# Kernel optimization log

Measured on AMD Instinct MI355X. Metric: run time of the kernel, lower is better.

The kernel has to match this reference:

```python
import jax, jax.numpy as jnp
import numpy as np

EPS = 1e-5
NUM_MP = 3

def _bn(x, gamma, beta):
    # eval-mode batch norm with running_mean=0, running_var=1
    return x * (gamma / jnp.sqrt(1.0 + EPS)) + beta

def _mlp(h, W1, b1, W2, b2):
    return jnp.maximum(h @ W1 + b1, 0.0) @ W2 + b2

def setup_inputs() -> dict:
    key = jax.random.key(0)
    ks = jax.random.split(key, 24)
    N, E, B, D = 50000, 800000, 16, 32
    inp = {
        'node_feats': jax.random.normal(ks[0], (N, D), jnp.float32),
        'edge_index': jax.random.randint(ks[1], (2, E), 0, N),
        'edge_feats': jax.random.normal(ks[2], (E, D), jnp.float32),
        'glob_feats': jax.random.normal(ks[3], (B, D), jnp.float32),
        'batch': jnp.sort(jax.random.randint(ks[4], (N,), 0, B)),
        'node_gamma': jax.random.uniform(ks[5], (D,), jnp.float32),
        'node_beta': jax.random.normal(ks[6], (D,), jnp.float32) * 0.1,
        'edge_gamma': jax.random.uniform(ks[7], (D,), jnp.float32),
        'edge_beta': jax.random.normal(ks[8], (D,), jnp.float32) * 0.1,
        'glob_gamma': jax.random.uniform(ks[9], (D,), jnp.float32),
        'glob_beta': jax.random.normal(ks[10], (D,), jnp.float32) * 0.1,
    }
    def w(k, shape):
        fan_in = shape[-2]
        return jax.random.normal(k, shape, jnp.float32) / np.sqrt(fan_in)
    inp['edge_W1'] = w(ks[11], (NUM_MP, 4 * D, 64)); inp['edge_b1'] = jnp.zeros((NUM_MP, 64))
    inp['edge_W2'] = w(ks[12], (NUM_MP, 64, D));     inp['edge_b2'] = jnp.zeros((NUM_MP, D))
    inp['node_W1'] = w(ks[13], (NUM_MP, 3 * D, 64)); inp['node_b1'] = jnp.zeros((NUM_MP, 64))
    inp['node_W2'] = w(ks[14], (NUM_MP, 64, D));     inp['node_b2'] = jnp.zeros((NUM_MP, D))
    inp['glob_W1'] = w(ks[15], (NUM_MP, 2 * D, 64)); inp['glob_b1'] = jnp.zeros((NUM_MP, 64))
    inp['glob_W2'] = w(ks[16], (NUM_MP, 64, D));     inp['glob_b2'] = jnp.zeros((NUM_MP, D))
    return inp

def reference(node_feats, edge_index, edge_feats, glob_feats, batch,
              node_gamma, node_beta, edge_gamma, edge_beta, glob_gamma, glob_beta,
              edge_W1, edge_b1, edge_W2, edge_b2,
              node_W1, node_b1, node_W2, node_b2,
              glob_W1, glob_b1, glob_W2, glob_b2):
    N = node_feats.shape[0]
    B = glob_feats.shape[0]
    src, dst = edge_index[0], edge_index[1]
    batch_src = batch[src]

    # input normalization
    x = _bn(node_feats, node_gamma, node_beta)
    e = _bn(edge_feats, edge_gamma, edge_beta)
    u = _bn(glob_feats, glob_gamma, glob_beta)

    # precompute mean-denominators (index structure is fixed)
    deg = jnp.maximum(jax.ops.segment_sum(jnp.ones_like(dst, jnp.float32), dst, num_segments=N), 1.0)[:, None]
    gcnt = jnp.maximum(jax.ops.segment_sum(jnp.ones_like(batch, jnp.float32), batch, num_segments=B), 1.0)[:, None]

    for l in range(NUM_MP):
        # edge model: MLP([x_src, x_dst, e, u[batch_src]])
        e_in = jnp.concatenate([x[src], x[dst], e, u[batch_src]], axis=-1)  # [E, 4D]
        e = _mlp(e_in, edge_W1[l], edge_b1[l], edge_W2[l], edge_b2[l])
        # node model: MLP([x, scatter_mean(e -> dst), u[batch]])
        agg = jax.ops.segment_sum(e, dst, num_segments=N) / deg  # [N, D]
        n_in = jnp.concatenate([x, agg, u[batch]], axis=-1)  # [N, 3D]
        x = _mlp(n_in, node_W1[l], node_b1[l], node_W2[l], node_b2[l])
        # global model: MLP([u, scatter_mean(x -> batch)])
        xg = jax.ops.segment_sum(x, batch, num_segments=B) / gcnt  # [B, D]
        g_in = jnp.concatenate([u, xg], axis=-1)  # [B, 2D]
        u = _mlp(g_in, glob_W1[l], glob_b1[l], glob_W2[l], glob_b2[l])
    return x, e, u
```

## Files before the change

kernel.cpp:

```cpp
#include <hip/hip_runtime.h>
#include <cstddef>

#define BN_RS 0.99999500003749971f

typedef __attribute__((ext_vector_type(8))) short bf16x8;
typedef __attribute__((ext_vector_type(4))) short bf16x4;
typedef __attribute__((ext_vector_type(4))) float f32x4;

#define LGKM0() asm volatile("s_waitcnt lgkmcnt(0)" ::: "memory")

__device__ __forceinline__ short f2bf(float f) {
    union { float f; unsigned u; } c; c.f = f;
    unsigned r = (c.u + 0x7fffu + ((c.u >> 16) & 1u)) >> 16;
    return (short)r;
}
__device__ __forceinline__ float bf2f(unsigned short h) {
    union { unsigned u; float f; } c; c.u = ((unsigned)h) << 16;
    return c.f;
}
__device__ __forceinline__ bf16x8 load8_bf(const float* __restrict__ p) {
    float4 a = *(const float4*)p;
    float4 b = *(const float4*)(p + 4);
    bf16x8 r;
    r[0] = f2bf(a.x); r[1] = f2bf(a.y); r[2] = f2bf(a.z); r[3] = f2bf(a.w);
    r[4] = f2bf(b.x); r[5] = f2bf(b.y); r[6] = f2bf(b.z); r[7] = f2bf(b.w);
    return r;
}

__global__ void bn_x_kernel(const float* __restrict__ in, const float* __restrict__ gamma,
                            const float* __restrict__ beta, unsigned short* __restrict__ xbf, int n4) {
    int i = blockIdx.x * blockDim.x + threadIdx.x;
    if (i >= n4) return;
    float4 v = ((const float4*)in)[i];
    float4 g = ((const float4*)gamma)[i & 7];
    float4 b = ((const float4*)beta)[i & 7];
    bf16x4 o;
    o[0] = f2bf(fmaf(v.x, g.x * BN_RS, b.x));
    o[1] = f2bf(fmaf(v.y, g.y * BN_RS, b.y));
    o[2] = f2bf(fmaf(v.z, g.z * BN_RS, b.z));
    o[3] = f2bf(fmaf(v.w, g.w * BN_RS, b.w));
    *(bf16x4*)(xbf + (size_t)i * 4) = o;
}

__global__ void bn_u_kernel(const float* __restrict__ in, const float* __restrict__ gamma,
                            const float* __restrict__ beta, float* __restrict__ ubuf,
                            unsigned short* __restrict__ ubf, int n4) {
    int i = blockIdx.x * blockDim.x + threadIdx.x;
    if (i >= n4) return;
    float4 v = ((const float4*)in)[i];
    float4 g = ((const float4*)gamma)[i & 7];
    float4 b = ((const float4*)beta)[i & 7];
    v.x = fmaf(v.x, g.x * BN_RS, b.x);
    v.y = fmaf(v.y, g.y * BN_RS, b.y);
    v.z = fmaf(v.z, g.z * BN_RS, b.z);
    v.w = fmaf(v.w, g.w * BN_RS, b.w);
    ((float4*)ubuf)[i] = v;
    bf16x4 o;
    o[0] = f2bf(v.x); o[1] = f2bf(v.y); o[2] = f2bf(v.z); o[3] = f2bf(v.w);
    *(bf16x4*)(ubf + (size_t)i * 4) = o;
}

__global__ void hist_kernel(const int* __restrict__ idx, int* __restrict__ cnt, int n) {
    int i = blockIdx.x * blockDim.x + threadIdx.x;
    if (i < n) atomicAdd(&cnt[idx[i]], 1);
}

__global__ void scan_kernel(const int* __restrict__ cnt, int* __restrict__ row, int N) {
    __shared__ int sd[1024];
    int tid = threadIdx.x;
    int chunk = (N + 1023) >> 10;
    int lo = tid * chunk, hi = min(lo + chunk, N);
    int s = 0;
    for (int i = lo; i < hi; ++i) s += cnt[i];
    sd[tid] = s;
    __syncthreads();
    for (int off = 1; off < 1024; off <<= 1) {
        int t = (tid >= off) ? sd[tid - off] : 0;
        __syncthreads();
        sd[tid] += t;
        __syncthreads();
    }
    int run = sd[tid] - s;
    for (int i = lo; i < hi; ++i) { row[i] = run; run += cnt[i]; }
    if (tid == 1023) row[N] = sd[1023];
}

__global__ void batch_src_kernel(const int* __restrict__ src, const int* __restrict__ batch,
                                 int* __restrict__ be, int E) {
    int e = blockIdx.x * blockDim.x + threadIdx.x;
    if (e < E) be[e] = batch[src[e]];
}

__global__ void scatter2_kernel(const int* __restrict__ src, const int* __restrict__ dst,
                                const int* __restrict__ bsrc, int* __restrict__ cursor,
                                int4* __restrict__ ip, int E) {
    int e = blockIdx.x * blockDim.x + threadIdx.x;
    if (e < E) {
        int d = dst[e];
        int slot = atomicAdd(&cursor[d], 1);
        ip[slot] = make_int4(src[e], d, bsrc[e], e);
    }
}

__global__ void prep_kernel(const float* __restrict__ eW1, const float* __restrict__ eW2,
                            const float* __restrict__ eb1,
                            const float* __restrict__ egam, const float* __restrict__ ebet,
                            unsigned short* __restrict__ w1p, unsigned short* __restrict__ w2p,
                            float* __restrict__ b1p) {
    int gid = blockIdx.x * 256 + threadIdx.x;
    if (gid < 24576) {
        int l = gid / 8192, r = gid % 8192;
        int s = r / 2048, r2 = r % 2048;
        int t = r2 / 512, r3 = r2 % 512;
        int lane = r3 / 8, j = r3 % 8;
        int q = lane >> 4, n = lane & 15;
        float w = eW1[(size_t)l * 8192 + (32 * s + 8 * q + j) * 64 + 16 * t + n];
        if (l == 0 && s == 2) w *= egam[8 * q + j] * BN_RS;
        w1p[gid] = (unsigned short)f2bf(w);
    } else if (gid < 24576 + 6144) {
        int g = gid - 24576;
        int l = g / 2048, r = g % 2048;
        int s = r / 1024, r2 = r % 1024;
        int t = r2 / 512, r3 = r2 % 512;
        int lane = r3 / 8, j = r3 % 8;
        int q = lane >> 4, n = lane & 15;
        w2p[g] = (unsigned short)f2bf(eW2[(size_t)l * 2048 + (32 * s + 8 * q + j) * 32 + 16 * t + n]);
    } else if (gid < 24576 + 6144 + 192) {
        int g = gid - 24576 - 6144;
        int l = g / 64, c = g % 64;
        float bb = eb1[l * 64 + c];
        if (l == 0) {
            for (int k = 0; k < 32; ++k) bb = fmaf(ebet[k], eW1[(64 + k) * 64 + c], bb);
        }
        b1p[g] = bb;
    }
}

__global__ __launch_bounds__(256, 4) void edge_mfma2(
    const unsigned short* __restrict__ xbf,
    const float* __restrict__ ef_raw,
    const unsigned short* __restrict__ ein,
    unsigned short* __restrict__ eout,
    float* __restrict__ eoutf,
    const unsigned short* __restrict__ ubf,
    const int4* __restrict__ ip,
    const unsigned short* __restrict__ w1p, const unsigned short* __restrict__ w2p,
    const float* __restrict__ b1p, const float* __restrict__ b2,
    int in0, int out2, int E) {
    __shared__ unsigned short w1lds[8192];
    __shared__ unsigned short hbuf[4][16 * 72];
    const int tid = threadIdx.x;
    const int wv = tid >> 6, lane = tid & 63;
    const int n = lane & 15, q = lane >> 4;

#pragma unroll
    for (int c = 0; c < 4; ++c)
        *(bf16x8*)(w1lds + c * 2048 + tid * 8) = *(const bf16x8*)(w1p + c * 2048 + tid * 8);

    bf16x8 w2f[2][2];
#pragma unroll
    for (int s = 0; s < 2; ++s)
#pragma unroll
        for (int t = 0; t < 2; ++t)
            w2f[s][t] = *(const bf16x8*)(w2p + ((s * 2 + t) * 64 + lane) * 8);
    float b1v[4];
#pragma unroll
    for (int t = 0; t < 4; ++t) b1v[t] = b1p[16 * t + n];
    float b2v[2];
#pragma unroll
    for (int t = 0; t < 2; ++t) b2v[t] = b2[16 * t + n];

    const int wbase = blockIdx.x * 256 + wv * 64;
    int4 ipt[4];
#pragma unroll
    for (int t = 0; t < 4; ++t) ipt[t] = ip[min(wbase + t * 16 + n, E - 1)];

    __syncthreads();

    bf16x8 g[2][4];
    auto load_tile = [&](int t4, bf16x8* af) {
        int4 p = ipt[t4];
        af[0] = *(const bf16x8*)(xbf + (size_t)p.x * 32 + 8 * q);
        af[1] = *(const bf16x8*)(xbf + (size_t)p.y * 32 + 8 * q);
        if (in0)
            af[2] = load8_bf(ef_raw + (size_t)p.w * 32 + 8 * q);
        else
            af[2] = *(const bf16x8*)(ein + (size_t)min(wbase + t4 * 16 + n, E - 1) * 32 + 8 * q);
        af[3] = *(const bf16x8*)(ubf + (size_t)p.z * 32 + 8 * q);
    };
    load_tile(0, g[0]);
    load_tile(1, g[1]);

    unsigned short* hw = hbuf[wv];
#pragma unroll
    for (int t4 = 0; t4 < 4; ++t4) {
        bf16x8* af = g[t4 & 1];

        f32x4 acc[4];
#pragma unroll
        for (int t = 0; t < 4; ++t) acc[t] = (f32x4){b1v[t], b1v[t], b1v[t], b1v[t]};
#pragma unroll
        for (int s = 0; s < 4; ++s)
#pragma unroll
            for (int t = 0; t < 4; ++t) {
                bf16x8 wf = *(const bf16x8*)(w1lds + (s * 4 + t) * 512 + lane * 8);
                acc[t] = __builtin_amdgcn_mfma_f32_16x16x32_bf16(af[s], wf, acc[t], 0, 0, 0);
            }

        if (t4 < 2) load_tile(t4 + 2, g[t4 & 1]);

        LGKM0();
#pragma unroll
        for (int t = 0; t < 4; ++t)
#pragma unroll
            for (int r = 0; r < 4; ++r)
                hw[(4 * q + r) * 72 + 16 * t + n] = (unsigned short)f2bf(fmaxf(acc[t][r], 0.0f));
        LGKM0();

        bf16x8 a2[2];
#pragma unroll
        for (int s = 0; s < 2; ++s)
            a2[s] = *(const bf16x8*)(hw + n * 72 + 32 * s + 8 * q);

        f32x4 acc2[2];
#pragma unroll
        for (int t = 0; t < 2; ++t) acc2[t] = (f32x4){b2v[t], b2v[t], b2v[t], b2v[t]};
#pragma unroll
        for (int s = 0; s < 2; ++s)
#pragma unroll
            for (int t = 0; t < 2; ++t)
                acc2[t] = __builtin_amdgcn_mfma_f32_16x16x32_bf16(a2[s], w2f[s][t], acc2[t], 0, 0, 0);

        const int rowbase = wbase + t4 * 16 + 4 * q;
#pragma unroll
        for (int t = 0; t < 2; ++t)
#pragma unroll
            for (int r = 0; r < 4; ++r) {
                int er = rowbase + r;
                if (er < E) eout[(size_t)er * 32 + 16 * t + n] = (unsigned short)f2bf(acc2[t][r]);
            }
        if (out2) {
            int ww[4];
#pragma unroll
            for (int r = 0; r < 4; ++r) ww[r] = __shfl(ipt[t4].w, 4 * q + r);
#pragma unroll
            for (int t = 0; t < 2; ++t)
#pragma unroll
                for (int r = 0; r < 4; ++r) {
                    int er = rowbase + r;
                    if (er < E) eoutf[(size_t)ww[r] * 32 + 16 * t + n] = acc2[t][r];
                }
        }
    }
}

__global__ void agg2_kernel(const int* __restrict__ row, const unsigned short* __restrict__ ebf,
                            float* __restrict__ aggf, int N) {
    int t = blockIdx.x * blockDim.x + threadIdx.x;
    int node = t >> 3;
    if (node >= N) return;
    int c = (t & 7) * 4;
    int s = row[node], e = row[node + 1];
    float a0 = 0.f, a1 = 0.f, a2 = 0.f, a3 = 0.f;
    for (int j = s; j < e; ++j) {
        ushort4 v = *(const ushort4*)(ebf + (size_t)j * 32 + c);
        a0 += bf2f(v.x); a1 += bf2f(v.y); a2 += bf2f(v.z); a3 += bf2f(v.w);
    }
    float inv = 1.0f / fmaxf((float)(e - s), 1.0f);
    float4 o = {a0 * inv, a1 * inv, a2 * inv, a3 * inv};
    *(float4*)(aggf + (size_t)node * 32 + c) = o;
}

__global__ __launch_bounds__(256) void node_mfma2(
    unsigned short* __restrict__ xbf, const float* __restrict__ aggf,
    const unsigned short* __restrict__ ubf, const int* __restrict__ batch,
    const float* __restrict__ W1, const float* __restrict__ b1,
    const float* __restrict__ W2, const float* __restrict__ b2,
    float* __restrict__ xf_out, int write_f32, int N) {
    __shared__ unsigned short hbuf[4][16 * 72];
    const int tid = threadIdx.x;
    const int wv = tid >> 6, lane = tid & 63;
    const int n = lane & 15, q = lane >> 4;

    bf16x8 w1f[3][4];
#pragma unroll
    for (int s = 0; s < 3; ++s)
#pragma unroll
        for (int t = 0; t < 4; ++t)
#pragma unroll
            for (int j = 0; j < 8; ++j)
                w1f[s][t][j] = f2bf(W1[(32 * s + 8 * q + j) * 64 + 16 * t + n]);
    bf16x8 w2f[2][2];
#pragma unroll
    for (int s = 0; s < 2; ++s)
#pragma unroll
        for (int t = 0; t < 2; ++t)
#pragma unroll
            for (int j = 0; j < 8; ++j)
                w2f[s][t][j] = f2bf(W2[(32 * s + 8 * q + j) * 32 + 16 * t + n]);
    float b1v[4];
#pragma unroll
    for (int t = 0; t < 4; ++t) b1v[t] = b1[16 * t + n];
    float b2v[2];
#pragma unroll
    for (int t = 0; t < 2; ++t) b2v[t] = b2[16 * t + n];

    const int base_n = blockIdx.x * 256 + wv * 64;

    auto load_tile = [&](int t4, bf16x8* af) {
        int nidx = min(base_n + t4 * 16 + n, N - 1);
        int bi = batch[nidx];
        af[0] = *(const bf16x8*)(xbf + (size_t)nidx * 32 + 8 * q);
        float4 a0 = *(const float4*)(aggf + (size_t)nidx * 32 + 8 * q);
        float4 a1 = *(const float4*)(aggf + (size_t)nidx * 32 + 8 * q + 4);
        bf16x8 agv;
        agv[0] = f2bf(a0.x); agv[1] = f2bf(a0.y); agv[2] = f2bf(a0.z); agv[3] = f2bf(a0.w);
        agv[4] = f2bf(a1.x); agv[5] = f2bf(a1.y); agv[6] = f2bf(a1.z); agv[7] = f2bf(a1.w);
        af[1] = agv;
        af[2] = *(const bf16x8*)(ubf + (size_t)bi * 32 + 8 * q);
    };

    unsigned short* hw = hbuf[wv];
    bf16x8 afb[2][3];
    load_tile(0, afb[0]);

#pragma unroll
    for (int t4 = 0; t4 < 4; ++t4) {
        bf16x8* af = afb[t4 & 1];
        if (t4 < 3) load_tile(t4 + 1, afb[(t4 + 1) & 1]);

        f32x4 acc[4];
#pragma unroll
        for (int t = 0; t < 4; ++t) acc[t] = (f32x4){b1v[t], b1v[t], b1v[t], b1v[t]};
#pragma unroll
        for (int s = 0; s < 3; ++s)
#pragma unroll
            for (int t = 0; t < 4; ++t)
                acc[t] = __builtin_amdgcn_mfma_f32_16x16x32_bf16(af[s], w1f[s][t], acc[t], 0, 0, 0);

        LGKM0();
#pragma unroll
        for (int t = 0; t < 4; ++t)
#pragma unroll
            for (int r = 0; r < 4; ++r)
                hw[(4 * q + r) * 72 + 16 * t + n] = (unsigned short)f2bf(fmaxf(acc[t][r], 0.0f));
        LGKM0();

        bf16x8 a2[2];
#pragma unroll
        for (int s = 0; s < 2; ++s)
            a2[s] = *(const bf16x8*)(hw + n * 72 + 32 * s + 8 * q);

        f32x4 acc2[2];
#pragma unroll
        for (int t = 0; t < 2; ++t) acc2[t] = (f32x4){b2v[t], b2v[t], b2v[t], b2v[t]};
#pragma unroll
        for (int s = 0; s < 2; ++s)
#pragma unroll
            for (int t = 0; t < 2; ++t)
                acc2[t] = __builtin_amdgcn_mfma_f32_16x16x32_bf16(a2[s], w2f[s][t], acc2[t], 0, 0, 0);

        int nrow = base_n + t4 * 16 + 4 * q;
#pragma unroll
        for (int t = 0; t < 2; ++t)
#pragma unroll
            for (int r = 0; r < 4; ++r) {
                int nr = nrow + r;
                if (nr < N) {
                    xbf[(size_t)nr * 32 + 16 * t + n] = (unsigned short)f2bf(acc2[t][r]);
                    if (write_f32) xf_out[(size_t)nr * 32 + 16 * t + n] = acc2[t][r];
                }
            }
    }
}

__global__ void xg_kernel(const unsigned short* __restrict__ xbf, const int* __restrict__ batch,
                          int N, float* __restrict__ xg) {
    int nblk = gridDim.x;
    int chunk = (N + nblk - 1) / nblk;
    int start = blockIdx.x * chunk;
    int end = min(start + chunk, N);
    int c = threadIdx.x & 31;
    int g = threadIdx.x >> 5;
    float acc = 0.0f;
    int cur = -1;
    for (int i = start + g; i < end; i += 8) {
        int b = batch[i];
        float v = bf2f(xbf[(size_t)i * 32 + c]);
        if (b != cur) {
            if (cur >= 0) atomicAdd(&xg[cur * 32 + c], acc);
            cur = b; acc = v;
        } else {
            acc += v;
        }
    }
    if (cur >= 0) atomicAdd(&xg[cur * 32 + c], acc);
}

__device__ __forceinline__ int lbound(const int* __restrict__ a, int nn, int v) {
    int lo = 0, hi = nn;
    while (lo < hi) {
        int mid = (lo + hi) >> 1;
        if (a[mid] < v) lo = mid + 1; else hi = mid;
    }
    return lo;
}

__global__ void glob_kernel(const float* __restrict__ u, const float* __restrict__ xg,
                            const int* __restrict__ batch, int N,
                            const float* __restrict__ W1, const float* __restrict__ b1,
                            const float* __restrict__ W2, const float* __restrict__ b2,
                            float* __restrict__ u_dst, unsigned short* __restrict__ ubf_dst) {
    int r = blockIdx.x;
    int t = threadIdx.x;
    __shared__ float gin[64];
    __shared__ float hs[64];
    __shared__ int cnts;
    if (t == 0) cnts = lbound(batch, N, r + 1) - lbound(batch, N, r);
    __syncthreads();
    if (t < 32)
        gin[t] = u[r * 32 + t];
    else
        gin[t] = xg[r * 32 + (t - 32)] / fmaxf((float)cnts, 1.0f);
    __syncthreads();
    float h = b1[t];
#pragma unroll
    for (int k = 0; k < 64; ++k) h = fmaf(gin[k], W1[k * 64 + t], h);
    hs[t] = fmaxf(h, 0.0f);
    __syncthreads();
    if (t < 32) {
        float o = b2[t];
#pragma unroll
        for (int k = 0; k < 64; ++k) o = fmaf(hs[k], W2[k * 32 + t], o);
        u_dst[r * 32 + t] = o;
        ubf_dst[r * 32 + t] = (unsigned short)f2bf(o);
    }
}

extern "C" void kernel_launch(void* const* d_in, const int* in_sizes, int n_in,
                              void* d_out, int out_size, void* d_ws, size_t ws_size,
                              hipStream_t stream) {
    const float* node_feats = (const float*)d_in[0];
    const int* edge_index = (const int*)d_in[1];
    const float* edge_feats = (const float*)d_in[2];
    const float* glob_feats = (const float*)d_in[3];
    const int* batch = (const int*)d_in[4];
    const float* node_gamma = (const float*)d_in[5];
    const float* node_beta = (const float*)d_in[6];
    const float* edge_gamma = (const float*)d_in[7];
    const float* edge_beta = (const float*)d_in[8];
    const float* glob_gamma = (const float*)d_in[9];
    const float* glob_beta = (const float*)d_in[10];
    const float* edge_W1 = (const float*)d_in[11];
    const float* edge_b1 = (const float*)d_in[12];
    const float* edge_W2 = (const float*)d_in[13];
    const float* edge_b2 = (const float*)d_in[14];
    const float* node_W1 = (const float*)d_in[15];
    const float* node_b1 = (const float*)d_in[16];
    const float* node_W2 = (const float*)d_in[17];
    const float* node_b2 = (const float*)d_in[18];
    const float* glob_W1 = (const float*)d_in[19];
    const float* glob_b1 = (const float*)d_in[20];
    const float* glob_W2 = (const float*)d_in[21];
    const float* glob_b2 = (const float*)d_in[22];

    const int N = in_sizes[0] / 32;
    const int E = in_sizes[1] / 2;
    const int B = in_sizes[3] / 32;

    float* x_out = (float*)d_out;
    float* e_out = x_out + (size_t)N * 32;
    float* u_out = e_out + (size_t)E * 32;

    char* ws = (char*)d_ws;
    unsigned short* x_bf = (unsigned short*)ws;  ws += (size_t)N * 32 * 2;
    float* aggf = (float*)ws;                    ws += (size_t)N * 32 * 4;
    unsigned short* u_bf = (unsigned short*)ws;  ws += 2048;
    float* u_buf = (float*)ws;                   ws += 4096;
    float* xg = (float*)ws;                      ws += 4096;
    int4* ip = (int4*)ws;                        ws += (size_t)E * 16;
    int* rowp = (int*)ws;                        ws += (size_t)(N + 4) * 4;
    int* cursor = (int*)ws;                      ws += (size_t)N * 4;
    int* hist = (int*)ws;                        ws += (size_t)N * 4;
    int* bsrc = (int*)ws;                        ws += (size_t)E * 4;
    unsigned short* w1p = (unsigned short*)ws;   ws += 24576 * 2;
    unsigned short* w2p = (unsigned short*)ws;   ws += 6144 * 2;
    float* b1p = (float*)ws;                     ws += 192 * 4;
    unsigned short* e_bf = (unsigned short*)ws;  ws += (size_t)E * 32 * 2;

    const int* ei_src = edge_index;
    const int* ei_dst = edge_index + E;

    bn_x_kernel<<<(N * 8 + 255) / 256, 256, 0, stream>>>(node_feats, node_gamma, node_beta, x_bf, N * 8);
    bn_u_kernel<<<(B * 8 + 255) / 256, 256, 0, stream>>>(glob_feats, glob_gamma, glob_beta, u_buf, u_bf, B * 8);
    prep_kernel<<<121, 256, 0, stream>>>(edge_W1, edge_W2, edge_b1, edge_gamma, edge_beta, w1p, w2p, b1p);

    hipMemsetAsync(hist, 0, (size_t)N * 4, stream);
    hist_kernel<<<(E + 255) / 256, 256, 0, stream>>>(ei_dst, hist, E);
    scan_kernel<<<1, 1024, 0, stream>>>(hist, rowp, N);
    hipMemcpyAsync(cursor, rowp, (size_t)N * 4, hipMemcpyDeviceToDevice, stream);
    batch_src_kernel<<<(E + 255) / 256, 256, 0, stream>>>(ei_src, batch, bsrc, E);
    scatter2_kernel<<<(E + 255) / 256, 256, 0, stream>>>(ei_src, ei_dst, bsrc, cursor, ip, E);

    for (int l = 0; l < 3; ++l) {
        hipMemsetAsync(xg, 0, (size_t)B * 32 * 4, stream);

        edge_mfma2<<<(E + 255) / 256, 256, 0, stream>>>(
            x_bf, edge_feats, e_bf, e_bf, e_out, u_bf, ip,
            w1p + (size_t)l * 8192, w2p + (size_t)l * 2048,
            b1p + l * 64, edge_b2 + l * 32,
            (l == 0) ? 1 : 0, (l == 2) ? 1 : 0, E);
        agg2_kernel<<<(N * 8 + 255) / 256, 256, 0, stream>>>(rowp, e_bf, aggf, N);
        node_mfma2<<<(N + 255) / 256, 256, 0, stream>>>(
            x_bf, aggf, u_bf, batch,
            node_W1 + (size_t)l * 96 * 64, node_b1 + l * 64,
            node_W2 + (size_t)l * 64 * 32, node_b2 + l * 32,
            x_out, (l == 2) ? 1 : 0, N);
        xg_kernel<<<256, 256, 0, stream>>>(x_bf, batch, N, xg);
        glob_kernel<<<B, 64, 0, stream>>>(
            u_buf, xg, batch, N,
            glob_W1 + (size_t)l * 64 * 64, glob_b1 + l * 64,
            glob_W2 + (size_t)l * 64 * 32, glob_b2 + l * 32,
            (l == 2) ? u_out : u_buf, u_bf);
    }
}
```

Measured before the change: 676.7 us.

## Swap MFMA operand order to keep hidden activations in registers, drop LDS staging

The edge and node MLP kernels now compute the transposed product (weights as A operand), so the first-layer accumulator layout, after a permutation folded into the W1 columns and biases, can be packed directly into bf16 A-fragments for the second MFMA. This removes the per-tile LDS round trip, its waitcnt fences and the scalar bf16 stores, and allows vectorized row-wise output stores. Preprocessing is also simplified: cursor init is fused into the scan, the batch[src] kernel is folded into the scatter, and aggregation uses 8-wide loads per thread. The risk is correctness of the hperm layout mapping and fewer threads per node in aggregation.

```diff
diff --git a/kernel.cpp b/kernel.cpp
--- a/kernel.cpp
+++ b/kernel.cpp
@@ -6,8 +6,6 @@
 typedef __attribute__((ext_vector_type(8))) short bf16x8;
 typedef __attribute__((ext_vector_type(4))) short bf16x4;
 typedef __attribute__((ext_vector_type(4))) float f32x4;
-
-#define LGKM0() asm volatile("s_waitcnt lgkmcnt(0)" ::: "memory")
 
 __device__ __forceinline__ short f2bf(float f) {
     union { float f; unsigned u; } c; c.f = f;
@@ -17,6 +15,11 @@
 __device__ __forceinline__ float bf2f(unsigned short h) {
     union { unsigned u; float f; } c; c.u = ((unsigned)h) << 16;
     return c.f;
+}
+__device__ __forceinline__ unsigned pk2bf(float a, float b) {
+    unsigned lo = (unsigned short)f2bf(a);
+    unsigned hi = (unsigned short)f2bf(b);
+    return lo | (hi << 16);
 }
 __device__ __forceinline__ bf16x8 load8_bf(const float* __restrict__ p) {
     float4 a = *(const float4*)p;
@@ -25,6 +28,22 @@
     r[0] = f2bf(a.x); r[1] = f2bf(a.y); r[2] = f2bf(a.z); r[3] = f2bf(a.w);
     r[4] = f2bf(b.x); r[5] = f2bf(b.y); r[6] = f2bf(b.z); r[7] = f2bf(b.w);
     return r;
+}
+
+__device__ __forceinline__ int hperm(int t, int m) {
+    return 32 * (t >> 1) + 8 * (m >> 2) + 4 * (t & 1) + (m & 3);
+}
+
+__device__ __forceinline__ void hpack(const f32x4* acc, bf16x8* a2) {
+#pragma unroll
+    for (int s = 0; s < 2; ++s) {
+        union { unsigned u[4]; bf16x8 v; } cvt;
+        cvt.u[0] = pk2bf(fmaxf(acc[2 * s][0], 0.0f), fmaxf(acc[2 * s][1], 0.0f));
+        cvt.u[1] = pk2bf(fmaxf(acc[2 * s][2], 0.0f), fmaxf(acc[2 * s][3], 0.0f));
+        cvt.u[2] = pk2bf(fmaxf(acc[2 * s + 1][0], 0.0f), fmaxf(acc[2 * s + 1][1], 0.0f));
+        cvt.u[3] = pk2bf(fmaxf(acc[2 * s + 1][2], 0.0f), fmaxf(acc[2 * s + 1][3], 0.0f));
+        a2[s] = cvt.v;
+    }
 }
 
 __global__ void bn_x_kernel(const float* __restrict__ in, const float* __restrict__ gamma,
@@ -65,7 +84,8 @@
     if (i < n) atomicAdd(&cnt[idx[i]], 1);
 }
 
-__global__ void scan_kernel(const int* __restrict__ cnt, int* __restrict__ row, int N) {
+__global__ void scan_kernel(const int* __restrict__ cnt, int* __restrict__ row,
+                            int* __restrict__ cursor, int N) {
     __shared__ int sd[1024];
     int tid = threadIdx.x;
     int chunk = (N + 1023) >> 10;
@@ -81,24 +101,19 @@
         __syncthreads();
     }
     int run = sd[tid] - s;
-    for (int i = lo; i < hi; ++i) { row[i] = run; run += cnt[i]; }
+    for (int i = lo; i < hi; ++i) { row[i] = run; cursor[i] = run; run += cnt[i]; }
     if (tid == 1023) row[N] = sd[1023];
 }
 
-__global__ void batch_src_kernel(const int* __restrict__ src, const int* __restrict__ batch,
-                                 int* __restrict__ be, int E) {
-    int e = blockIdx.x * blockDim.x + threadIdx.x;
-    if (e < E) be[e] = batch[src[e]];
-}
-
 __global__ void scatter2_kernel(const int* __restrict__ src, const int* __restrict__ dst,
-                                const int* __restrict__ bsrc, int* __restrict__ cursor,
+                                const int* __restrict__ batch, int* __restrict__ cursor,
                                 int4* __restrict__ ip, int E) {
     int e = blockIdx.x * blockDim.x + threadIdx.x;
     if (e < E) {
         int d = dst[e];
+        int sv = src[e];
         int slot = atomicAdd(&cursor[d], 1);
-        ip[slot] = make_int4(src[e], d, bsrc[e], e);
+        ip[slot] = make_int4(sv, d, batch[sv], e);
     }
 }
 
@@ -114,7 +129,7 @@
         int t = r2 / 512, r3 = r2 % 512;
         int lane = r3 / 8, j = r3 % 8;
         int q = lane >> 4, n = lane & 15;
-        float w = eW1[(size_t)l * 8192 + (32 * s + 8 * q + j) * 64 + 16 * t + n];
+        float w = eW1[(size_t)l * 8192 + (32 * s + 8 * q + j) * 64 + hperm(t, n)];
         if (l == 0 && s == 2) w *= egam[8 * q + j] * BN_RS;
         w1p[gid] = (unsigned short)f2bf(w);
     } else if (gid < 24576 + 6144) {
@@ -136,7 +151,7 @@
     }
 }
 
-__global__ __launch_bounds__(256, 4) void edge_mfma2(
+__global__ __launch_bounds__(256, 4) void edge_mfma3(
     const unsigned short* __restrict__ xbf,
     const float* __restrict__ ef_raw,
     const unsigned short* __restrict__ ein,
@@ -148,9 +163,8 @@
     const float* __restrict__ b1p, const float* __restrict__ b2,
     int in0, int out2, int E) {
     __shared__ unsigned short w1lds[8192];
-    __shared__ unsigned short hbuf[4][16 * 72];
     const int tid = threadIdx.x;
-    const int wv = tid >> 6, lane = tid & 63;
+    const int lane = tid & 63;
     const int n = lane & 15, q = lane >> 4;
 
 #pragma unroll
@@ -163,14 +177,15 @@
 #pragma unroll
         for (int t = 0; t < 2; ++t)
             w2f[s][t] = *(const bf16x8*)(w2p + ((s * 2 + t) * 64 + lane) * 8);
-    float b1v[4];
-#pragma unroll
-    for (int t = 0; t < 4; ++t) b1v[t] = b1p[16 * t + n];
-    float b2v[2];
-#pragma unroll
-    for (int t = 0; t < 2; ++t) b2v[t] = b2[16 * t + n];
-
-    const int wbase = blockIdx.x * 256 + wv * 64;
+    f32x4 b1v[4];
+#pragma unroll
+    for (int t = 0; t < 4; ++t)
+        b1v[t] = *(const f32x4*)(b1p + 32 * (t >> 1) + 8 * q + 4 * (t & 1));
+    f32x4 b2v[2];
+#pragma unroll
+    for (int t = 0; t < 2; ++t) b2v[t] = *(const f32x4*)(b2 + 16 * t + 4 * q);
+
+    const int wbase = blockIdx.x * 256 + (tid >> 6) * 64;
     int4 ipt[4];
 #pragma unroll
     for (int t = 0; t < 4; ++t) ipt[t] = ip[min(wbase + t * 16 + n, E - 1)];
@@ -191,65 +206,50 @@
     load_tile(0, g[0]);
     load_tile(1, g[1]);
 
-    unsigned short* hw = hbuf[wv];
 #pragma unroll
     for (int t4 = 0; t4 < 4; ++t4) {
         bf16x8* af = g[t4 & 1];
 
         f32x4 acc[4];
 #pragma unroll
-        for (int t = 0; t < 4; ++t) acc[t] = (f32x4){b1v[t], b1v[t], b1v[t], b1v[t]};
+        for (int t = 0; t < 4; ++t) acc[t] = b1v[t];
 #pragma unroll
         for (int s = 0; s < 4; ++s)
 #pragma unroll
             for (int t = 0; t < 4; ++t) {
                 bf16x8 wf = *(const bf16x8*)(w1lds + (s * 4 + t) * 512 + lane * 8);
-                acc[t] = __builtin_amdgcn_mfma_f32_16x16x32_bf16(af[s], wf, acc[t], 0, 0, 0);
+                acc[t] = __builtin_amdgcn_mfma_f32_16x16x32_bf16(wf, af[s], acc[t], 0, 0, 0);
             }
 
         if (t4 < 2) load_tile(t4 + 2, g[t4 & 1]);
 
-        LGKM0();
-#pragma unroll
-        for (int t = 0; t < 4; ++t)
-#pragma unroll
-            for (int r = 0; r < 4; ++r)
-                hw[(4 * q + r) * 72 + 16 * t + n] = (unsigned short)f2bf(fmaxf(acc[t][r], 0.0f));
-        LGKM0();
-
         bf16x8 a2[2];
+        hpack(acc, a2);
+
+        f32x4 acc2[2];
+#pragma unroll
+        for (int t = 0; t < 2; ++t) acc2[t] = b2v[t];
 #pragma unroll
         for (int s = 0; s < 2; ++s)
-            a2[s] = *(const bf16x8*)(hw + n * 72 + 32 * s + 8 * q);
-
-        f32x4 acc2[2];
-#pragma unroll
-        for (int t = 0; t < 2; ++t) acc2[t] = (f32x4){b2v[t], b2v[t], b2v[t], b2v[t]};
-#pragma unroll
-        for (int s = 0; s < 2; ++s)
 #pragma unroll
             for (int t = 0; t < 2; ++t)
-                acc2[t] = __builtin_amdgcn_mfma_f32_16x16x32_bf16(a2[s], w2f[s][t], acc2[t], 0, 0, 0);
-
-        const int rowbase = wbase + t4 * 16 + 4 * q;
-#pragma unroll
-        for (int t = 0; t < 2; ++t)
-#pragma unroll
-            for (int r = 0; r < 4; ++r) {
-                int er = rowbase + r;
-                if (er < E) eout[(size_t)er * 32 + 16 * t + n] = (unsigned short)f2bf(acc2[t][r]);
+                acc2[t] = __builtin_amdgcn_mfma_f32_16x16x32_bf16(w2f[s][t], a2[s], acc2[t], 0, 0, 0);
+
+        int e = wbase + t4 * 16 + n;
+        if (e < E) {
+#pragma unroll
+            for (int t = 0; t < 2; ++t) {
+                uint2 pkd;
+                pkd.x = pk2bf(acc2[t][0], acc2[t][1]);
+                pkd.y = pk2bf(acc2[t][2], acc2[t][3]);
+                *(uint2*)(eout + (size_t)e * 32 + 16 * t + 4 * q) = pkd;
             }
-        if (out2) {
-            int ww[4];
-#pragma unroll
-            for (int r = 0; r < 4; ++r) ww[r] = __shfl(ipt[t4].w, 4 * q + r);
-#pragma unroll
-            for (int t = 0; t < 2; ++t)
-#pragma unroll
-                for (int r = 0; r < 4; ++r) {
-                    int er = rowbase + r;
-                    if (er < E) eoutf[(size_t)ww[r] * 32 + 16 * t + n] = acc2[t][r];
-                }
+            if (out2) {
+                int ww = ipt[t4].w;
+#pragma unroll
+                for (int t = 0; t < 2; ++t)
+                    *(f32x4*)(eoutf + (size_t)ww * 32 + 16 * t + 4 * q) = acc2[t];
+            }
         }
     }
 }
@@ -257,29 +257,31 @@
 __global__ void agg2_kernel(const int* __restrict__ row, const unsigned short* __restrict__ ebf,
                             float* __restrict__ aggf, int N) {
     int t = blockIdx.x * blockDim.x + threadIdx.x;
-    int node = t >> 3;
+    int node = t >> 2;
     if (node >= N) return;
-    int c = (t & 7) * 4;
+    int c = (t & 3) * 8;
     int s = row[node], e = row[node + 1];
-    float a0 = 0.f, a1 = 0.f, a2 = 0.f, a3 = 0.f;
+    float a[8] = {0.f, 0.f, 0.f, 0.f, 0.f, 0.f, 0.f, 0.f};
     for (int j = s; j < e; ++j) {
-        ushort4 v = *(const ushort4*)(ebf + (size_t)j * 32 + c);
-        a0 += bf2f(v.x); a1 += bf2f(v.y); a2 += bf2f(v.z); a3 += bf2f(v.w);
+        bf16x8 v = *(const bf16x8*)(ebf + (size_t)j * 32 + c);
+#pragma unroll
+        for (int k = 0; k < 8; ++k) a[k] += bf2f((unsigned short)v[k]);
     }
     float inv = 1.0f / fmaxf((float)(e - s), 1.0f);
-    float4 o = {a0 * inv, a1 * inv, a2 * inv, a3 * inv};
-    *(float4*)(aggf + (size_t)node * 32 + c) = o;
-}
-
-__global__ __launch_bounds__(256) void node_mfma2(
+    float4 o0 = {a[0] * inv, a[1] * inv, a[2] * inv, a[3] * inv};
+    float4 o1 = {a[4] * inv, a[5] * inv, a[6] * inv, a[7] * inv};
+    *(float4*)(aggf + (size_t)node * 32 + c) = o0;
+    *(float4*)(aggf + (size_t)node * 32 + c + 4) = o1;
+}
+
+__global__ __launch_bounds__(256) void node_mfma3(
     unsigned short* __restrict__ xbf, const float* __restrict__ aggf,
     const unsigned short* __restrict__ ubf, const int* __restrict__ batch,
     const float* __restrict__ W1, const float* __restrict__ b1,
     const float* __restrict__ W2, const float* __restrict__ b2,
     float* __restrict__ xf_out, int write_f32, int N) {
-    __shared__ unsigned short hbuf[4][16 * 72];
     const int tid = threadIdx.x;
-    const int wv = tid >> 6, lane = tid & 63;
+    const int lane = tid & 63;
     const int n = lane & 15, q = lane >> 4;
 
     bf16x8 w1f[3][4];
@@ -289,7 +291,7 @@
         for (int t = 0; t < 4; ++t)
 #pragma unroll
             for (int j = 0; j < 8; ++j)
-                w1f[s][t][j] = f2bf(W1[(32 * s + 8 * q + j) * 64 + 16 * t + n]);
+                w1f[s][t][j] = f2bf(W1[(32 * s + 8 * q + j) * 64 + hperm(t, n)]);
     bf16x8 w2f[2][2];
 #pragma unroll
     for (int s = 0; s < 2; ++s)
@@ -298,14 +300,15 @@
 #pragma unroll
             for (int j = 0; j < 8; ++j)
                 w2f[s][t][j] = f2bf(W2[(32 * s + 8 * q + j) * 32 + 16 * t + n]);
-    float b1v[4];
-#pragma unroll
-    for (int t = 0; t < 4; ++t) b1v[t] = b1[16 * t + n];
-    float b2v[2];
-#pragma unroll
-    for (int t = 0; t < 2; ++t) b2v[t] = b2[16 * t + n];
-
-    const int base_n = blockIdx.x * 256 + wv * 64;
+    f32x4 b1v[4];
+#pragma unroll
+    for (int t = 0; t < 4; ++t)
+        b1v[t] = *(const f32x4*)(b1 + 32 * (t >> 1) + 8 * q + 4 * (t & 1));
+    f32x4 b2v[2];
+#pragma unroll
+    for (int t = 0; t < 2; ++t) b2v[t] = *(const f32x4*)(b2 + 16 * t + 4 * q);
+
+    const int base_n = blockIdx.x * 256 + (tid >> 6) * 64;
 
     auto load_tile = [&](int t4, bf16x8* af) {
         int nidx = min(base_n + t4 * 16 + n, N - 1);
@@ -320,7 +323,6 @@
         af[2] = *(const bf16x8*)(ubf + (size_t)bi * 32 + 8 * q);
     };
 
-    unsigned short* hw = hbuf[wv];
     bf16x8 afb[2][3];
     load_tile(0, afb[0]);
 
@@ -331,46 +333,40 @@
 
         f32x4 acc[4];
 #pragma unroll
-        for (int t = 0; t < 4; ++t) acc[t] = (f32x4){b1v[t], b1v[t], b1v[t], b1v[t]};
+        for (int t = 0; t < 4; ++t) acc[t] = b1v[t];
 #pragma unroll
         for (int s = 0; s < 3; ++s)
 #pragma unroll
             for (int t = 0; t < 4; ++t)
-                acc[t] = __builtin_amdgcn_mfma_f32_16x16x32_bf16(af[s], w1f[s][t], acc[t], 0, 0, 0);
-
-        LGKM0();
-#pragma unroll
-        for (int t = 0; t < 4; ++t)
-#pragma unroll
-            for (int r = 0; r < 4; ++r)
-                hw[(4 * q + r) * 72 + 16 * t + n] = (unsigned short)f2bf(fmaxf(acc[t][r], 0.0f));
-        LGKM0();
+                acc[t] = __builtin_amdgcn_mfma_f32_16x16x32_bf16(w1f[s][t], af[s], acc[t], 0, 0, 0);
 
         bf16x8 a2[2];
+        hpack(acc, a2);
+
+        f32x4 acc2[2];
+#pragma unroll
+        for (int t = 0; t < 2; ++t) acc2[t] = b2v[t];
 #pragma unroll
         for (int s = 0; s < 2; ++s)
-            a2[s] = *(const bf16x8*)(hw + n * 72 + 32 * s + 8 * q);
-
-        f32x4 acc2[2];
-#pragma unroll
-        for (int t = 0; t < 2; ++t) acc2[t] = (f32x4){b2v[t], b2v[t], b2v[t], b2v[t]};
-#pragma unroll
-        for (int s = 0; s < 2; ++s)
 #pragma unroll
             for (int t = 0; t < 2; ++t)
-                acc2[t] = __builtin_amdgcn_mfma_f32_16x16x32_bf16(a2[s], w2f[s][t], acc2[t], 0, 0, 0);
-
-        int nrow = base_n + t4 * 16 + 4 * q;
-#pragma unroll
-        for (int t = 0; t < 2; ++t)
-#pragma unroll
-            for (int r = 0; r < 4; ++r) {
-                int nr = nrow + r;
-                if (nr < N) {
-                    xbf[(size_t)nr * 32 + 16 * t + n] = (unsigned short)f2bf(acc2[t][r]);
-                    if (write_f32) xf_out[(size_t)nr * 32 + 16 * t + n] = acc2[t][r];
-                }
+                acc2[t] = __builtin_amdgcn_mfma_f32_16x16x32_bf16(w2f[s][t], a2[s], acc2[t], 0, 0, 0);
+
+        int nd = base_n + t4 * 16 + n;
+        if (nd < N) {
+#pragma unroll
+            for (int t = 0; t < 2; ++t) {
+                uint2 pkd;
+                pkd.x = pk2bf(acc2[t][0], acc2[t][1]);
+                pkd.y = pk2bf(acc2[t][2], acc2[t][3]);
+                *(uint2*)(xbf + (size_t)nd * 32 + 16 * t + 4 * q) = pkd;
             }
+            if (write_f32) {
+#pragma unroll
+                for (int t = 0; t < 2; ++t)
+                    *(f32x4*)(xf_out + (size_t)nd * 32 + 16 * t + 4 * q) = acc2[t];
+            }
+        }
     }
 }
 
@@ -482,7 +478,6 @@
     int* rowp = (int*)ws;                        ws += (size_t)(N + 4) * 4;
     int* cursor = (int*)ws;                      ws += (size_t)N * 4;
     int* hist = (int*)ws;                        ws += (size_t)N * 4;
-    int* bsrc = (int*)ws;                        ws += (size_t)E * 4;
     unsigned short* w1p = (unsigned short*)ws;   ws += 24576 * 2;
     unsigned short* w2p = (unsigned short*)ws;   ws += 6144 * 2;
     float* b1p = (float*)ws;                     ws += 192 * 4;
@@ -497,21 +492,19 @@
 
     hipMemsetAsync(hist, 0, (size_t)N * 4, stream);
     hist_kernel<<<(E + 255) / 256, 256, 0, stream>>>(ei_dst, hist, E);
-    scan_kernel<<<1, 1024, 0, stream>>>(hist, rowp, N);
-    hipMemcpyAsync(cursor, rowp, (size_t)N * 4, hipMemcpyDeviceToDevice, stream);
-    batch_src_kernel<<<(E + 255) / 256, 256, 0, stream>>>(ei_src, batch, bsrc, E);
-    scatter2_kernel<<<(E + 255) / 256, 256, 0, stream>>>(ei_src, ei_dst, bsrc, cursor, ip, E);
+    scan_kernel<<<1, 1024, 0, stream>>>(hist, rowp, cursor, N);
+    scatter2_kernel<<<(E + 255) / 256, 256, 0, stream>>>(ei_src, ei_dst, batch, cursor, ip, E);
 
     for (int l = 0; l < 3; ++l) {
         hipMemsetAsync(xg, 0, (size_t)B * 32 * 4, stream);
 
-        edge_mfma2<<<(E + 255) / 256, 256, 0, stream>>>(
+        edge_mfma3<<<(E + 255) / 256, 256, 0, stream>>>(
             x_bf, edge_feats, e_bf, e_bf, e_out, u_bf, ip,
             w1p + (size_t)l * 8192, w2p + (size_t)l * 2048,
             b1p + l * 64, edge_b2 + l * 32,
             (l == 0) ? 1 : 0, (l == 2) ? 1 : 0, E);
-        agg2_kernel<<<(N * 8 + 255) / 256, 256, 0, stream>>>(rowp, e_bf, aggf, N);
-        node_mfma2<<<(N + 255) / 256, 256, 0, stream>>>(
+        agg2_kernel<<<(N * 4 + 255) / 256, 256, 0, stream>>>(rowp, e_bf, aggf, N);
+        node_mfma3<<<(N + 255) / 256, 256, 0, stream>>>(
             x_bf, aggf, u_bf, batch,
             node_W1 + (size_t)l * 96 * 64, node_b1 + l * 64,
             node_W2 + (size_t)l * 64 * 32, node_b2 + l * 32,
```

Measured after the change: 1.017 ms. +50.3%, slower.
